# Kernel optimization log

Measured on AMD Instinct MI355X. Metric: run time of the kernel, lower is better.

Reference implementation:

```python
import jax, jax.numpy as jnp
import numpy as np
from jax import lax

N, CIN, H, W = 128, 1024, 14, 14
CF, TH = 128, 128          # cv_filter, te_hidden
HP, GT, FP, A = 256, 256, 256, 32


def setup_inputs() -> dict:
    key = jax.random.key(0)
    ks = jax.random.split(key, 12)
    s = 0.05
    return {
        "image": jax.random.normal(ks[0], (N, CIN, H, W), jnp.float32),
        "code": jax.random.normal(ks[1], (N, TH), jnp.float32),
        "conv_w": jax.random.normal(ks[2], (CF, CIN, 3, 3), jnp.float32) * 0.02,
        "conv_b": jnp.zeros((CF,), jnp.float32),
        "hp_w0": jax.random.normal(ks[3], (CF + 2 + TH, HP), jnp.float32) * s,
        "hp_b0": jnp.zeros((HP,), jnp.float32),
        "hp_w1": jax.random.normal(ks[4], (HP, 1), jnp.float32) * s,
        "hp_b1": jnp.zeros((1,), jnp.float32),
        "gt_w0": jax.random.normal(ks[5], ((CF + 2) * 2 + TH, GT), jnp.float32) * s,
        "gt_b0": jnp.zeros((GT,), jnp.float32),
        "gt_w1": jax.random.normal(ks[6], (GT, GT), jnp.float32) * s,
        "gt_b1": jnp.zeros((GT,), jnp.float32),
        "fp_w0": jax.random.normal(ks[7], (GT, FP), jnp.float32) * s,
        "fp_b0": jnp.zeros((FP,), jnp.float32),
        "fp_w1": jax.random.normal(ks[8], (FP, A), jnp.float32) * s,
        "fp_b1": jnp.zeros((A,), jnp.float32),
    }


def _sarn(image, code, conv_w, conv_b, hp_w0, hp_b0, hp_w1, hp_b1,
          gt_w0, gt_b0, gt_w1, gt_b1, fp_w0, fp_b0, fp_w1, fp_b1):
    # visual_resize: 3x3 conv, stride 1, pad 1 (NCHW)
    x = lax.conv_general_dilated(image, conv_w, (1, 1), "SAME",
                                 dimension_numbers=("NCHW", "OIHW", "NCHW"))
    x = x + conv_b[None, :, None, None]                       # [n, cf, h, w]
    n, c, h, w = x.shape
    o = h * w
    # sarn_encode: append x/y coordinate channels and question code
    xc = jnp.broadcast_to(jnp.linspace(-1.0, 1.0, h).reshape(1, 1, h, 1), (n, 1, h, w))
    yc = jnp.broadcast_to(jnp.linspace(-1.0, 1.0, w).reshape(1, 1, 1, w), (n, 1, h, w))
    coord = jnp.concatenate([x, xc, yc], axis=1)              # [n, cf+2, h, w]
    q = jnp.broadcast_to(code[:, :, None, None], (n, code.shape[1], h, w))
    qenc = jnp.concatenate([coord, q], axis=1)                # [n, cf+2+th, h, w]
    ce = coord.reshape(n, c + 2, o).transpose(0, 2, 1)        # [n, o, cf+2]
    qe = qenc.reshape(n, -1, o).transpose(0, 2, 1)            # [n, o, cf+2+th]
    # h_psi: per-object attention logit
    a = jax.nn.relu(jnp.einsum("nod,dh->noh", qe, hp_w0) + hp_b0)
    att = jnp.einsum("noh,hk->nok", a, hp_w1) + hp_b1         # [n, o, 1]
    # sarn_pair: softmax select a single soft object, pair with every object
    sel = jax.nn.softmax(att[..., 0], axis=1)                 # [n, o]
    selected = jnp.einsum("no,nod->nd", sel, ce)              # [n, cf+2]
    pairs = jnp.concatenate(
        [qe, jnp.broadcast_to(selected[:, None, :], ce.shape)], axis=2)  # [n, o, 2*(cf+2)+th]
    # g_theta MLP + sum over objects
    g = jax.nn.relu(jnp.einsum("nop,pg->nog", pairs, gt_w0) + gt_b0)
    g = jax.nn.relu(jnp.einsum("nog,gk->nok", g, gt_w1) + gt_b1)
    relations = g.sum(axis=1)                                 # [n, gt]
    # f_phi MLP -> answer logits
    f = jax.nn.relu(relations @ fp_w0 + fp_b0)
    return f @ fp_w1 + fp_b1                                  # [n, a_size]


def reference(image, code, conv_w, conv_b, hp_w0, hp_b0, hp_w1, hp_b1,
              gt_w0, gt_b0, gt_w1, gt_b1, fp_w0, fp_b0, fp_w1, fp_b1):
    return _sarn(image, code, conv_w, conv_b, hp_w0, hp_b0, hp_w1, hp_b1,
                 gt_w0, gt_b0, gt_w1, gt_b1, fp_w0, fp_b0, fp_w1, fp_b1)
```

## Files before the change

kernel.cpp:

```cpp
#include <hip/hip_runtime.h>
#include <stdint.h>

typedef unsigned short u16;
typedef __bf16 bf16x8 __attribute__((ext_vector_type(8)));
typedef float f32x4 __attribute__((ext_vector_type(4)));

__device__ __forceinline__ u16 f2b(float f) {
  union { float f; uint32_t u; } v; v.f = f;
  uint32_t r = v.u + 0x7fffu + ((v.u >> 16) & 1u);
  return (u16)(r >> 16);
}
__device__ __forceinline__ float b2f(u16 b) {
  union { float f; uint32_t u; } v; v.u = ((uint32_t)b) << 16;
  return v.f;
}
__device__ __forceinline__ void g2l16(const void* g, void* l) {
  __builtin_amdgcn_global_load_lds(
      (const __attribute__((address_space(1))) void*)g,
      (__attribute__((address_space(3))) void*)l, 16, 0, 0);
}

#define N_SAMP 128
#define OPAD   224
#define ROWS   (N_SAMP * OPAD)

__global__ __launch_bounds__(256) void prep_weights(
    const float* __restrict__ conv_w, const float* __restrict__ hp_w0,
    const float* __restrict__ gt_w0, const float* __restrict__ gt_w1,
    u16* __restrict__ W2, u16* __restrict__ hp_w0t,
    u16* __restrict__ gt_w0t, u16* __restrict__ gt_w1t) {
  int idx = blockIdx.x * 256 + threadIdx.x;
  const int nW2 = 9 * 128 * 1024;
  const int nHP = 256 * 288;
  const int nGT0 = 256 * 288;
  const int nGT1 = 256 * 256;
  if (idx < nW2) {
    int s = idx / 131072; int r = idx & 131071;
    int cf = r >> 10; int cin = r & 1023;
    W2[idx] = f2b(conv_w[(cf * 1024 + cin) * 9 + s]);
    return;
  }
  idx -= nW2;
  if (idx < nHP) {
    int nn = idx / 288, kk = idx % 288;
    hp_w0t[nn * 288 + kk] = (kk < 258) ? f2b(hp_w0[kk * 256 + nn]) : (u16)0;
    return;
  }
  idx -= nHP;
  if (idx < nGT0) {
    int nn = idx / 288, kk = idx % 288;
    gt_w0t[nn * 288 + kk] = (kk < 258) ? f2b(gt_w0[kk * 256 + nn]) : (u16)0;
    return;
  }
  idx -= nGT0;
  if (idx < nGT1) {
    int nn = idx >> 8, kk = idx & 255;
    gt_w1t[nn * 256 + kk] = f2b(gt_w1[kk * 256 + nn]);
  }
}

__global__ __launch_bounds__(256) void prep_img(const float* __restrict__ image,
                                                u16* __restrict__ imgT) {
  __shared__ float t[64][197];
  int n = blockIdx.x >> 4;
  int cin0 = (blockIdx.x & 15) * 64;
  const float* src = image + ((size_t)n * 1024 + cin0) * 196;
  for (int e = threadIdx.x; e < 64 * 196; e += 256) {
    int c = e / 196, sp = e % 196;
    t[c][sp] = src[c * 196 + sp];
  }
  __syncthreads();
  int w = threadIdx.x >> 6, lane = threadIdx.x & 63;
  for (int i = 0; i < 64; ++i) {
    int spg = i * 4 + w;
    int gy = spg >> 4, gx = spg & 15;
    float v = 0.f;
    if (gy >= 1 && gy <= 14 && gx >= 1 && gx <= 14) v = t[lane][(gy - 1) * 14 + (gx - 1)];
    imgT[(((size_t)(n * 256 + spg)) << 10) + cin0 + lane] = f2b(v);
  }
}

__global__ __launch_bounds__(256) void fill_qe(const float* __restrict__ code,
                                               u16* __restrict__ qeb) {
  int base = blockIdx.x * 8;
  for (int rr = 0; rr < 8; ++rr) {
    int r = base + rr;
    int n = r / 224, o = r % 224;
    int y = o / 14, x = o % 14;
    bool valid = o < 196;
    u16* row = qeb + (size_t)r * 288;
    for (int c = threadIdx.x; c < 288; c += 256) {
      u16 v;
      if (c < 128) { if (valid) continue; v = 0; }
      else if (c == 128) v = valid ? f2b(-1.f + 2.f * y / 13.f) : (u16)0;
      else if (c == 129) v = valid ? f2b(-1.f + 2.f * x / 13.f) : (u16)0;
      else if (c < 258) v = valid ? f2b(code[n * 128 + (c - 130)]) : (u16)0;
      else v = 0;
      row[c] = v;
    }
  }
}

__global__ __launch_bounds__(256) void conv_gemm(
    const u16* __restrict__ imgT, const u16* __restrict__ W2,
    float* __restrict__ convAcc) {
  __shared__ __align__(16) u16 lA[2][128 * 64];
  __shared__ __align__(16) u16 lB[2][128 * 64];
  int tid = threadIdx.x, lane = tid & 63, w = tid >> 6;
  int wg = blockIdx.x;
  int xcd = wg & 7, grp = wg >> 3;
  int n = ((grp / 6) << 3) | xcd;
  int r6 = grp % 6;
  int oh = r6 / 3, ks = r6 % 3;
  int oBase = oh * 112;
  size_t nBase = (size_t)n << 8;
  int rowIn = lane >> 3;
  int cA = ((lane & 7) ^ rowIn) << 3;

  int yxA[4];
  for (int ii = 0; ii < 4; ++ii) {
    int t = w + ii * 4;
    int o = oBase + t * 8 + rowIn;
    bool valid = (o < 196) && (t < 14);
    int y = o / 14, x = o - y * 14;
    yxA[ii] = valid ? (y * 16 + x) : 0;
  }

  f32x4 acc[7][2];
#pragma unroll
  for (int mt = 0; mt < 7; ++mt)
#pragma unroll
    for (int j = 0; j < 2; ++j) acc[mt][j] = (f32x4){0.f, 0.f, 0.f, 0.f};

  int l = lane & 15, q = lane >> 4;

  auto STAGE = [&](int buf, int si, int k0) {
    int off = ks * 16 + si;
    const u16* Ws = W2 + ((size_t)((ks * 3 + si) * 128) << 10);
#pragma unroll
    for (int ii = 0; ii < 4; ++ii)
      g2l16(imgT + ((nBase + (size_t)(yxA[ii] + off)) << 10) + k0 + cA,
            &lA[buf][(w + ii * 4) * 512]);
#pragma unroll
    for (int ii = 0; ii < 4; ++ii)
      g2l16(Ws + ((size_t)((w + ii * 4) * 8 + rowIn) << 10) + k0 + cA,
            &lB[buf][(w + ii * 4) * 512]);
  };

  auto COMPUTE = [&](int cur) {
#pragma unroll
    for (int kk = 0; kk < 2; ++kk) {
      int co = ((((kk << 2) | q) ^ (l & 7)) << 3);
      bf16x8 af[7];
#pragma unroll
      for (int mt = 0; mt < 7; ++mt)
        af[mt] = *(const bf16x8*)&lA[cur][(mt * 16 + l) * 64 + co];
#pragma unroll
      for (int jj = 0; jj < 2; ++jj) {
        bf16x8 bb = *(const bf16x8*)&lB[cur][(w * 32 + jj * 16 + l) * 64 + co];
#pragma unroll
        for (int mt = 0; mt < 7; ++mt)
          acc[mt][jj] = __builtin_amdgcn_mfma_f32_16x16x32_bf16(af[mt], bb, acc[mt][jj], 0, 0, 0);
      }
    }
  };

  STAGE(0, 0, 0);
#pragma unroll 2
  for (int it = 0; it < 47; ++it) {
    int nxt = it + 1;
    STAGE(nxt & 1, nxt >> 4, (nxt & 15) << 6);
    asm volatile("s_waitcnt vmcnt(8)" ::: "memory");
    __builtin_amdgcn_s_barrier();
    __builtin_amdgcn_sched_barrier(0);
    COMPUTE(it & 1);
    __builtin_amdgcn_sched_barrier(0);
    __builtin_amdgcn_s_barrier();
    __builtin_amdgcn_sched_barrier(0);
  }
  asm volatile("s_waitcnt vmcnt(0)" ::: "memory");
  __builtin_amdgcn_s_barrier();
  __builtin_amdgcn_sched_barrier(0);
  COMPUTE(1);

#pragma unroll
  for (int mt = 0; mt < 7; ++mt) {
    int o = oBase + mt * 16 + q * 4;
#pragma unroll
    for (int r4 = 0; r4 < 4; ++r4) {
      if (o + r4 < 196) {
        float* dst = convAcc + (size_t)(n * 224 + o + r4) * 128 + w * 32 + l;
        atomicAdd(dst, acc[mt][0][r4]);
        atomicAdd(dst + 16, acc[mt][1][r4]);
      }
    }
  }
}

__global__ __launch_bounds__(256) void conv_fix(
    const float* __restrict__ convAcc, const float* __restrict__ conv_b,
    u16* __restrict__ qeb) {
  int idx = blockIdx.x * 256 + threadIdx.x;
  int row196 = idx >> 5;
  int c0 = (idx & 31) << 2;
  int n = row196 / 196, o = row196 - n * 196;
  size_t row = (size_t)(n * 224 + o);
  const float4 v = *(const float4*)(convAcc + (row << 7) + c0);
  const float4 b = *(const float4*)(conv_b + c0);
  ushort4 pk;
  pk.x = f2b(v.x + b.x); pk.y = f2b(v.y + b.y);
  pk.z = f2b(v.z + b.z); pk.w = f2b(v.w + b.w);
  *(ushort4*)(qeb + row * 288 + c0) = pk;
}

template <int MODE, int KP, int KC>
__global__ __launch_bounds__(256) void gemm_kernel(
    const u16* __restrict__ A, const u16* __restrict__ Bt,
    const float* __restrict__ bias, const float* __restrict__ vec,
    float* __restrict__ outF, u16* __restrict__ outB) {
  __shared__ __align__(16) u16 lA[2][128 * 32];
  __shared__ __align__(16) u16 lB[2][128 * 32];
  int tid = threadIdx.x, lane = tid & 63, w = tid >> 6;
  int bx = blockIdx.x, by = blockIdx.y;
  int r0 = bx * 112;
  int cBase = by * 128;
  int kb = (((lane & 3) ^ ((lane >> 3) & 3)) << 3);
  int rA0 = r0 + w * 16 + (lane >> 2);
  int rA1 = r0 + (w + 4) * 16 + (lane >> 2);
  const u16* gA0 = A + (size_t)rA0 * KP + kb;
  const u16* gA1 = A + (size_t)rA1 * KP + kb;
  int cB0 = cBase + w * 16 + (lane >> 2);
  int cB1 = cBase + (w + 4) * 16 + (lane >> 2);
  const u16* gB0 = Bt + (size_t)cB0 * KP + kb;
  const u16* gB1 = Bt + (size_t)cB1 * KP + kb;

  f32x4 acc[7][2];
#pragma unroll
  for (int mt = 0; mt < 7; ++mt)
#pragma unroll
    for (int j = 0; j < 2; ++j) acc[mt][j] = (f32x4){0.f, 0.f, 0.f, 0.f};
  int colW = w * 32;
  int l = lane & 15, q = lane >> 4;
  int co = ((q ^ ((l >> 1) & 3)) << 3);

  auto STAGE = [&](int buf, int cb) {
    g2l16(gA0 + cb * 32, &lA[buf][w * 512]);
    g2l16(gA1 + cb * 32, &lA[buf][(w + 4) * 512]);
    g2l16(gB0 + cb * 32, &lB[buf][w * 512]);
    g2l16(gB1 + cb * 32, &lB[buf][(w + 4) * 512]);
  };

  auto COMPUTE = [&](int cur) {
    bf16x8 af[7];
#pragma unroll
    for (int mt = 0; mt < 7; ++mt)
      af[mt] = *(const bf16x8*)&lA[cur][(mt * 16 + l) * 32 + co];
#pragma unroll
    for (int j = 0; j < 2; ++j) {
      bf16x8 bfr = *(const bf16x8*)&lB[cur][(colW + j * 16 + l) * 32 + co];
#pragma unroll
      for (int mt = 0; mt < 7; ++mt)
        acc[mt][j] = __builtin_amdgcn_mfma_f32_16x16x32_bf16(af[mt], bfr, acc[mt][j], 0, 0, 0);
    }
  };

  STAGE(0, 0);
#pragma unroll
  for (int it = 0; it < KC - 1; ++it) {
    STAGE((it & 1) ^ 1, it + 1);
    asm volatile("s_waitcnt vmcnt(4)" ::: "memory");
    __builtin_amdgcn_s_barrier();
    __builtin_amdgcn_sched_barrier(0);
    COMPUTE(it & 1);
    __builtin_amdgcn_sched_barrier(0);
    __builtin_amdgcn_s_barrier();
    __builtin_amdgcn_sched_barrier(0);
  }
  asm volatile("s_waitcnt vmcnt(0)" ::: "memory");
  __builtin_amdgcn_s_barrier();
  __builtin_amdgcn_sched_barrier(0);
  COMPUTE((KC - 1) & 1);

  int q4 = lane >> 4, c = lane & 15;
  if (MODE == 0) {
    float attp[7][4];
#pragma unroll
    for (int mt = 0; mt < 7; ++mt)
#pragma unroll
      for (int r = 0; r < 4; ++r) attp[mt][r] = 0.f;
#pragma unroll
    for (int j = 0; j < 2; ++j) {
      int col = cBase + colW + j * 16 + c;
      float b0 = bias[col], w1 = vec[col];
#pragma unroll
      for (int mt = 0; mt < 7; ++mt)
#pragma unroll
        for (int r = 0; r < 4; ++r) {
          float v = fmaxf(acc[mt][j][r] + b0, 0.f);
          attp[mt][r] += v * w1;
        }
    }
#pragma unroll
    for (int mt = 0; mt < 7; ++mt)
#pragma unroll
      for (int r = 0; r < 4; ++r) {
        float p = attp[mt][r];
        p += __shfl_xor(p, 1, 64);
        p += __shfl_xor(p, 2, 64);
        p += __shfl_xor(p, 4, 64);
        p += __shfl_xor(p, 8, 64);
        if (c == 0) atomicAdd(&outF[r0 + mt * 16 + q4 * 4 + r], p);
      }
  } else if (MODE == 1) {
    int n = bx >> 1;
#pragma unroll
    for (int mt = 0; mt < 7; ++mt)
#pragma unroll
      for (int j = 0; j < 2; ++j) {
        int col = cBase + colW + j * 16 + c;
        float b = bias[n * 256 + col];
#pragma unroll
        for (int r = 0; r < 4; ++r) {
          int row = r0 + mt * 16 + q4 * 4 + r;
          outB[(size_t)row * 256 + col] = f2b(fmaxf(acc[mt][j][r] + b, 0.f));
        }
      }
  } else {
    int n = bx >> 1;
    int ob = (bx & 1) * 112;
#pragma unroll
    for (int j = 0; j < 2; ++j) {
      int col = cBase + colW + j * 16 + c;
      float b = bias[col];
      float sum = 0.f;
#pragma unroll
      for (int mt = 0; mt < 7; ++mt)
#pragma unroll
        for (int r = 0; r < 4; ++r) {
          int o = ob + mt * 16 + q4 * 4 + r;
          if (o < 196) sum += fmaxf(acc[mt][j][r] + b, 0.f);
        }
      sum += __shfl_xor(sum, 16, 64);
      sum += __shfl_xor(sum, 32, 64);
      if (q4 == 0) atomicAdd(&outF[n * 256 + col], sum);
    }
  }
}

__global__ __launch_bounds__(256) void sel_kernel(
    const float* __restrict__ att, const u16* __restrict__ qeb,
    const float* __restrict__ gt_w0, const float* __restrict__ gt_b0,
    float* __restrict__ bias2) {
  int n = blockIdx.x, t = threadIdx.x;
  int w = t >> 6, lane = t & 63;
  __shared__ u16 sq[196][130];
  __shared__ float sm[196];
  __shared__ float sel[130];
  __shared__ float red[8];
  const u16* base = qeb + (size_t)n * 224 * 288;
  for (int o = w; o < 196; o += 4) {
    const u16* rowp = base + (size_t)o * 288;
    for (int c = lane; c < 130; c += 64) sq[o][c] = rowp[c];
  }
  float a = (t < 196) ? att[n * 224 + t] : -1e30f;
  float m = a;
  for (int mask = 1; mask < 64; mask <<= 1) m = fmaxf(m, __shfl_xor(m, mask, 64));
  if (lane == 0) red[w] = m;
  __syncthreads();
  float M = fmaxf(fmaxf(red[0], red[1]), fmaxf(red[2], red[3]));
  float e = (t < 196) ? expf(a - M) : 0.f;
  float sAcc = e;
  for (int mask = 1; mask < 64; mask <<= 1) sAcc += __shfl_xor(sAcc, mask, 64);
  if (lane == 0) red[4 + w] = sAcc;
  __syncthreads();
  float S = red[4] + red[5] + red[6] + red[7];
  if (t < 196) sm[t] = e / S;
  __syncthreads();
  if (t < 130) {
    float acc = 0.f;
    for (int o = 0; o < 196; ++o) acc += sm[o] * b2f(sq[o][t]);
    sel[t] = acc;
  }
  __syncthreads();
  float acc2 = gt_b0[t];
  for (int d = 0; d < 130; ++d) acc2 += sel[d] * gt_w0[(258 + d) * 256 + t];
  bias2[n * 256 + t] = acc2;
}

__global__ __launch_bounds__(256) void fphi(
    const float* __restrict__ relations, const float* __restrict__ fp_w0,
    const float* __restrict__ fp_b0, const float* __restrict__ fp_w1,
    const float* __restrict__ fp_b1, float* __restrict__ out) {
  int n = blockIdx.x, t = threadIdx.x;
  __shared__ float rel[256];
  __shared__ float f[256];
  rel[t] = relations[n * 256 + t];
  __syncthreads();
  float acc = fp_b0[t];
  for (int k = 0; k < 256; ++k) acc += rel[k] * fp_w0[k * 256 + t];
  f[t] = fmaxf(acc, 0.f);
  __syncthreads();
  if (t < 32) {
    float o = fp_b1[0];
    for (int k = 0; k < 256; ++k) o += f[k] * fp_w1[k * 32 + t];
    out[n * 32 + t] = o;
  }
}

extern "C" void kernel_launch(void* const* d_in, const int* in_sizes, int n_in,
                              void* d_out, int out_size, void* d_ws, size_t ws_size,
                              hipStream_t stream) {
  const float* image = (const float*)d_in[0];
  const float* code = (const float*)d_in[1];
  const float* conv_w = (const float*)d_in[2];
  const float* conv_b = (const float*)d_in[3];
  const float* hp_w0 = (const float*)d_in[4];
  const float* hp_b0 = (const float*)d_in[5];
  const float* hp_w1 = (const float*)d_in[6];
  const float* gt_w0 = (const float*)d_in[8];
  const float* gt_b0 = (const float*)d_in[9];
  const float* gt_w1 = (const float*)d_in[10];
  const float* gt_b1 = (const float*)d_in[11];
  const float* fp_w0 = (const float*)d_in[12];
  const float* fp_b0 = (const float*)d_in[13];
  const float* fp_w1 = (const float*)d_in[14];
  const float* fp_b1 = (const float*)d_in[15];
  float* out = (float*)d_out;

  char* p = (char*)d_ws;
  u16* imgT = (u16*)p;   p += (size_t)128 * 256 * 1024 * 2;
  u16* W2 = (u16*)p;     p += (size_t)9 * 128 * 1024 * 2;
  u16* qeb = (u16*)p;    p += (size_t)ROWS * 288 * 2;
  u16* hp_w0t = (u16*)p; p += (size_t)256 * 288 * 2;
  u16* gt_w0t = (u16*)p; p += (size_t)256 * 288 * 2;
  u16* gt_w1t = (u16*)p; p += (size_t)256 * 256 * 2;
  float* att = (float*)p;   p += (size_t)ROWS * 4;
  float* bias2 = (float*)p; p += (size_t)128 * 256 * 4;
  float* convAcc = (float*)p; p += (size_t)ROWS * 128 * 4;
  float* relations = (float*)p; p += (size_t)128 * 256 * 4;
  u16* g1 = (u16*)convAcc;

  hipMemsetAsync(att, 0, (size_t)ROWS * 4, stream);
  hipMemsetAsync(relations, 0, (size_t)128 * 256 * 4, stream);
  hipMemsetAsync(convAcc, 0, (size_t)ROWS * 128 * 4, stream);

  prep_weights<<<5440, 256, 0, stream>>>(conv_w, hp_w0, gt_w0, gt_w1, W2, hp_w0t, gt_w0t, gt_w1t);
  prep_img<<<2048, 256, 0, stream>>>(image, imgT);
  fill_qe<<<ROWS / 8, 256, 0, stream>>>(code, qeb);
  conv_gemm<<<768, 256, 0, stream>>>(imgT, W2, convAcc);
  conv_fix<<<3136, 256, 0, stream>>>(convAcc, conv_b, qeb);
  gemm_kernel<0, 288, 9><<<dim3(256, 2), 256, 0, stream>>>(qeb, hp_w0t, hp_b0, hp_w1, att, nullptr);
  sel_kernel<<<128, 256, 0, stream>>>(att, qeb, gt_w0, gt_b0, bias2);
  gemm_kernel<1, 288, 9><<<dim3(256, 2), 256, 0, stream>>>(qeb, gt_w0t, bias2, nullptr, nullptr, g1);
  gemm_kernel<2, 256, 8><<<dim3(256, 2), 256, 0, stream>>>(g1, gt_w1t, gt_b1, nullptr, relations, nullptr);
  fphi<<<128, 256, 0, stream>>>(relations, fp_w0, fp_b0, fp_w1, fp_b1, out);
}
```

Baseline: 425.7 us.

## Rework conv GEMM into 4-slot K32 pipeline with 2-way split-K

Restructures the implicit-GEMM conv kernel. The old version used a double-buffered K=64 stage across 3 tap splits (768 blocks). The new one uses a 4-slot ring of K=32 half-stages with three loads in flight, a 2-way split over the 288 half-steps (512 blocks), a new LDS swizzle, and 32-bit offset arithmetic. LDS fragment reads are issued before the next stage's loads and barrier, and MFMAs run at raised priority, so memory latency overlaps compute. The cost is more barriers per unit of K work and fewer blocks, which may lower occupancy and load balance. Fewer atomic partial-sum writes are needed.

```diff
diff --git a/kernel.cpp b/kernel.cpp
--- a/kernel.cpp
+++ b/kernel.cpp
@@ -104,26 +104,28 @@
 __global__ __launch_bounds__(256) void conv_gemm(
     const u16* __restrict__ imgT, const u16* __restrict__ W2,
     float* __restrict__ convAcc) {
-  __shared__ __align__(16) u16 lA[2][128 * 64];
-  __shared__ __align__(16) u16 lB[2][128 * 64];
+  __shared__ __align__(16) u16 lA[4 * 4096];
+  __shared__ __align__(16) u16 lB[4 * 4096];
   int tid = threadIdx.x, lane = tid & 63, w = tid >> 6;
   int wg = blockIdx.x;
   int xcd = wg & 7, grp = wg >> 3;
-  int n = ((grp / 6) << 3) | xcd;
-  int r6 = grp % 6;
-  int oh = r6 / 3, ks = r6 % 3;
+  int n = ((grp >> 2) << 3) | xcd;
+  int r4g = grp & 3;
+  int oh = r4g >> 1, ks = r4g & 1;
   int oBase = oh * 112;
-  size_t nBase = (size_t)n << 8;
-  int rowIn = lane >> 3;
-  int cA = ((lane & 7) ^ rowIn) << 3;
-
-  int yxA[4];
-  for (int ii = 0; ii < 4; ++ii) {
+  int nBase = n << 8;
+  int rowIn = lane >> 2;
+  int swz = (((lane & 3) ^ ((lane >> 3) & 3)) << 3);
+
+  int aLane[2], bLane[2];
+  for (int ii = 0; ii < 2; ++ii) {
     int t = w + ii * 4;
-    int o = oBase + t * 8 + rowIn;
-    bool valid = (o < 196) && (t < 14);
+    int o = oBase + t * 16 + rowIn;
+    bool valid = (o < 196) && (t < 7);
     int y = o / 14, x = o - y * 14;
-    yxA[ii] = valid ? (y * 16 + x) : 0;
+    int yx = valid ? (y * 16 + x) : 0;
+    aLane[ii] = (yx << 10) + swz;
+    bLane[ii] = ((t * 16 + rowIn) << 10) + swz;
   }
 
   f32x4 acc[7][2];
@@ -133,55 +135,64 @@
     for (int j = 0; j < 2; ++j) acc[mt][j] = (f32x4){0.f, 0.f, 0.f, 0.f};
 
   int l = lane & 15, q = lane >> 4;
-
-  auto STAGE = [&](int buf, int si, int k0) {
-    int off = ks * 16 + si;
-    const u16* Ws = W2 + ((size_t)((ks * 3 + si) * 128) << 10);
-#pragma unroll
-    for (int ii = 0; ii < 4; ++ii)
-      g2l16(imgT + ((nBase + (size_t)(yxA[ii] + off)) << 10) + k0 + cA,
-            &lA[buf][(w + ii * 4) * 512]);
-#pragma unroll
-    for (int ii = 0; ii < 4; ++ii)
-      g2l16(Ws + ((size_t)((w + ii * 4) * 8 + rowIn) << 10) + k0 + cA,
-            &lB[buf][(w + ii * 4) * 512]);
+  int co = ((q ^ ((l >> 1) & 3)) << 3);
+  int hBase = ks * 144;
+
+  auto STAGE = [&](int slot, int h) {
+    int hg = hBase + h;
+    int s = hg >> 1;
+    int tap = s >> 4, cb = s & 15, kk = hg & 1;
+    int colb = (cb << 6) + (kk << 5);
+    int d3 = tap / 3;
+    int aScal = ((nBase + d3 * 16 + (tap - d3 * 3)) << 10) + colb;
+    int bScal = ((tap << 17) ) + colb;
+#pragma unroll
+    for (int ii = 0; ii < 2; ++ii)
+      g2l16(imgT + (size_t)aScal + aLane[ii], &lA[slot * 4096 + (w + ii * 4) * 512]);
+#pragma unroll
+    for (int ii = 0; ii < 2; ++ii)
+      g2l16(W2 + (size_t)bScal + bLane[ii], &lB[slot * 4096 + (w + ii * 4) * 512]);
   };
 
-  auto COMPUTE = [&](int cur) {
-#pragma unroll
-    for (int kk = 0; kk < 2; ++kk) {
-      int co = ((((kk << 2) | q) ^ (l & 7)) << 3);
-      bf16x8 af[7];
-#pragma unroll
-      for (int mt = 0; mt < 7; ++mt)
-        af[mt] = *(const bf16x8*)&lA[cur][(mt * 16 + l) * 64 + co];
-#pragma unroll
-      for (int jj = 0; jj < 2; ++jj) {
-        bf16x8 bb = *(const bf16x8*)&lB[cur][(w * 32 + jj * 16 + l) * 64 + co];
-#pragma unroll
-        for (int mt = 0; mt < 7; ++mt)
-          acc[mt][jj] = __builtin_amdgcn_mfma_f32_16x16x32_bf16(af[mt], bb, acc[mt][jj], 0, 0, 0);
-      }
-    }
-  };
-
-  STAGE(0, 0, 0);
-#pragma unroll 2
-  for (int it = 0; it < 47; ++it) {
-    int nxt = it + 1;
-    STAGE(nxt & 1, nxt >> 4, (nxt & 15) << 6);
-    asm volatile("s_waitcnt vmcnt(8)" ::: "memory");
-    __builtin_amdgcn_s_barrier();
-    __builtin_amdgcn_sched_barrier(0);
-    COMPUTE(it & 1);
-    __builtin_amdgcn_sched_barrier(0);
-    __builtin_amdgcn_s_barrier();
-    __builtin_amdgcn_sched_barrier(0);
-  }
-  asm volatile("s_waitcnt vmcnt(0)" ::: "memory");
+  STAGE(0, 0);
+  STAGE(1, 1);
+  STAGE(2, 2);
+  asm volatile("s_waitcnt vmcnt(8)" ::: "memory");
   __builtin_amdgcn_s_barrier();
   __builtin_amdgcn_sched_barrier(0);
-  COMPUTE(1);
+
+#pragma unroll 4
+  for (int h = 0; h < 144; ++h) {
+    int slot = h & 3;
+    const u16* aS = lA + slot * 4096;
+    const u16* bS = lB + slot * 4096;
+    bf16x8 af[7], bb0, bb1;
+#pragma unroll
+    for (int mt = 0; mt < 7; ++mt)
+      af[mt] = *(const bf16x8*)&aS[(mt * 16 + l) * 32 + co];
+    bb0 = *(const bf16x8*)&bS[(w * 32 + l) * 32 + co];
+    bb1 = *(const bf16x8*)&bS[(w * 32 + 16 + l) * 32 + co];
+    if (h <= 140) {
+      STAGE((h + 3) & 3, h + 3);
+      asm volatile("s_waitcnt vmcnt(8)" ::: "memory");
+    } else {
+      asm volatile("s_waitcnt vmcnt(0)" ::: "memory");
+    }
+    __builtin_amdgcn_s_barrier();
+    asm volatile("s_waitcnt lgkmcnt(0)" ::: "memory");
+    __builtin_amdgcn_sched_barrier(0);
+    __builtin_amdgcn_s_setprio(1);
+#pragma unroll
+    for (int mt = 0; mt < 7; ++mt)
+      acc[mt][0] = __builtin_amdgcn_mfma_f32_16x16x32_bf16(af[mt], bb0, acc[mt][0], 0, 0, 0);
+#pragma unroll
+    for (int mt = 0; mt < 7; ++mt)
+      acc[mt][1] = __builtin_amdgcn_mfma_f32_16x16x32_bf16(af[mt], bb1, acc[mt][1], 0, 0, 0);
+    __builtin_amdgcn_s_setprio(0);
+    __builtin_amdgcn_sched_barrier(0);
+    __builtin_amdgcn_s_barrier();
+    __builtin_amdgcn_sched_barrier(0);
+  }
 
 #pragma unroll
   for (int mt = 0; mt < 7; ++mt) {
@@ -447,7 +458,7 @@
   prep_weights<<<5440, 256, 0, stream>>>(conv_w, hp_w0, gt_w0, gt_w1, W2, hp_w0t, gt_w0t, gt_w1t);
   prep_img<<<2048, 256, 0, stream>>>(image, imgT);
   fill_qe<<<ROWS / 8, 256, 0, stream>>>(code, qeb);
-  conv_gemm<<<768, 256, 0, stream>>>(imgT, W2, convAcc);
+  conv_gemm<<<512, 256, 0, stream>>>(imgT, W2, convAcc);
   conv_fix<<<3136, 256, 0, stream>>>(convAcc, conv_b, qeb);
   gemm_kernel<0, 288, 9><<<dim3(256, 2), 256, 0, stream>>>(qeb, hp_w0t, hp_b0, hp_w1, att, nullptr);
   sel_kernel<<<128, 256, 0, stream>>>(att, qeb, gt_w0, gt_b0, bias2);
```

Measured after the change: 423.4 us. No clear change (-0.5%).

## Restructure conv GEMM to reuse padded image tile across all nine taps

Applied to the files above, without the earlier changes.

The conv implicit-GEMM now loads the whole padded 16x16 image plane for a 32-channel slice into LDS once and reuses it for all 9 filter taps by shifting the row offset. Only weight tiles are streamed, through a 4-slot ring. Each block covers all 196 output positions and all 128 filters, and the work is split 4 ways along input channels instead of 3 ways by tap, so the grid drops from 768 to 512 blocks. This is meant to cut redundant image loads from global memory. In exchange there are more atomic adds per block, one barrier per 32-wide k step, and a hand-tuned waitcnt schedule that is fragile.

```diff
diff --git a/kernel.cpp b/kernel.cpp
--- a/kernel.cpp
+++ b/kernel.cpp
@@ -104,94 +104,116 @@
 __global__ __launch_bounds__(256) void conv_gemm(
     const u16* __restrict__ imgT, const u16* __restrict__ W2,
     float* __restrict__ convAcc) {
-  __shared__ __align__(16) u16 lA[2][128 * 64];
-  __shared__ __align__(16) u16 lB[2][128 * 64];
+  __shared__ __align__(16) u16 lA[2][256 * 32];
+  __shared__ __align__(16) u16 lB[4][128 * 32];
   int tid = threadIdx.x, lane = tid & 63, w = tid >> 6;
   int wg = blockIdx.x;
-  int xcd = wg & 7, grp = wg >> 3;
-  int n = ((grp / 6) << 3) | xcd;
-  int r6 = grp % 6;
-  int oh = r6 / 3, ks = r6 % 3;
-  int oBase = oh * 112;
+  int xcd = wg & 7;
+  int ks = xcd >> 1;
+  int n = ((wg >> 3) << 1) | (xcd & 1);
+  int kbase = ks << 3;
   size_t nBase = (size_t)n << 8;
-  int rowIn = lane >> 3;
-  int cA = ((lane & 7) ^ rowIn) << 3;
-
-  int yxA[4];
-  for (int ii = 0; ii < 4; ++ii) {
-    int t = w + ii * 4;
-    int o = oBase + t * 8 + rowIn;
-    bool valid = (o < 196) && (t < 14);
+  int wm = w >> 1, wn = w & 1;
+  int rowIn = lane >> 2;
+  int swz = (((lane & 3) ^ ((rowIn >> 1) & 3)) << 3);
+
+  int l = lane & 15, q = lane >> 4;
+
+  int posB[7];
+#pragma unroll
+  for (int mt = 0; mt < 7; ++mt) {
+    int o = wm * 112 + mt * 16 + l;
     int y = o / 14, x = o - y * 14;
-    yxA[ii] = valid ? (y * 16 + x) : 0;
-  }
-
-  f32x4 acc[7][2];
+    posB[mt] = (o < 196) ? (y * 16 + x) : 0;
+  }
+
+  f32x4 acc[7][4];
 #pragma unroll
   for (int mt = 0; mt < 7; ++mt)
 #pragma unroll
-    for (int j = 0; j < 2; ++j) acc[mt][j] = (f32x4){0.f, 0.f, 0.f, 0.f};
-
-  int l = lane & 15, q = lane >> 4;
-
-  auto STAGE = [&](int buf, int si, int k0) {
-    int off = ks * 16 + si;
-    const u16* Ws = W2 + ((size_t)((ks * 3 + si) * 128) << 10);
-#pragma unroll
-    for (int ii = 0; ii < 4; ++ii)
-      g2l16(imgT + ((nBase + (size_t)(yxA[ii] + off)) << 10) + k0 + cA,
-            &lA[buf][(w + ii * 4) * 512]);
-#pragma unroll
-    for (int ii = 0; ii < 4; ++ii)
-      g2l16(Ws + ((size_t)((w + ii * 4) * 8 + rowIn) << 10) + k0 + cA,
-            &lB[buf][(w + ii * 4) * 512]);
+    for (int j = 0; j < 4; ++j) acc[mt][j] = (f32x4){0.f, 0.f, 0.f, 0.f};
+
+  auto STAGE_A = [&](int buf, int cbg) {
+    int k0 = cbg << 5;
+#pragma unroll
+    for (int ii = 0; ii < 4; ++ii) {
+      int r = w * 64 + ii * 16;
+      g2l16(imgT + ((nBase + (size_t)(r + rowIn)) << 10) + k0 + swz,
+            &lA[buf][r * 32]);
+    }
   };
-
-  auto COMPUTE = [&](int cur) {
-#pragma unroll
-    for (int kk = 0; kk < 2; ++kk) {
-      int co = ((((kk << 2) | q) ^ (l & 7)) << 3);
-      bf16x8 af[7];
-#pragma unroll
-      for (int mt = 0; mt < 7; ++mt)
-        af[mt] = *(const bf16x8*)&lA[cur][(mt * 16 + l) * 64 + co];
-#pragma unroll
-      for (int jj = 0; jj < 2; ++jj) {
-        bf16x8 bb = *(const bf16x8*)&lB[cur][(w * 32 + jj * 16 + l) * 64 + co];
-#pragma unroll
-        for (int mt = 0; mt < 7; ++mt)
-          acc[mt][jj] = __builtin_amdgcn_mfma_f32_16x16x32_bf16(af[mt], bb, acc[mt][jj], 0, 0, 0);
-      }
+  auto STAGE_B = [&](int slot, int ss) {
+    int cbg = kbase + ss / 9;
+    int tp = ss - (ss / 9) * 9;
+    int k0 = cbg << 5;
+    const u16* Ws = W2 + (((size_t)tp * 128) << 10);
+#pragma unroll
+    for (int ii = 0; ii < 2; ++ii) {
+      int c = w * 32 + ii * 16;
+      g2l16(Ws + ((size_t)(c + rowIn) << 10) + k0 + swz, &lB[slot][c * 32]);
     }
   };
 
-  STAGE(0, 0, 0);
-#pragma unroll 2
-  for (int it = 0; it < 47; ++it) {
-    int nxt = it + 1;
-    STAGE(nxt & 1, nxt >> 4, (nxt & 15) << 6);
-    asm volatile("s_waitcnt vmcnt(8)" ::: "memory");
+  STAGE_A(0, kbase);
+  STAGE_B(0, 0);
+  STAGE_B(1, 1);
+
+  int tap = 0, tapOff = 0, cb = 0;
+#pragma unroll 1
+  for (int s = 0; s < 72; ++s) {
+    if (s + 2 < 72) STAGE_B((s + 2) & 3, s + 2);
+    if (tap == 7 && cb < 7) STAGE_A((cb + 1) & 1, kbase + cb + 1);
+    if (s < 68) {
+      if (tap >= 7) asm volatile("s_waitcnt vmcnt(8)" ::: "memory");
+      else          asm volatile("s_waitcnt vmcnt(4)" ::: "memory");
+    } else if (s < 70) {
+      asm volatile("s_waitcnt vmcnt(4)" ::: "memory");
+    } else if (s == 70) {
+      asm volatile("s_waitcnt vmcnt(2)" ::: "memory");
+    } else {
+      asm volatile("s_waitcnt vmcnt(0)" ::: "memory");
+    }
     __builtin_amdgcn_s_barrier();
     __builtin_amdgcn_sched_barrier(0);
-    COMPUTE(it & 1);
-    __builtin_amdgcn_sched_barrier(0);
-    __builtin_amdgcn_s_barrier();
-    __builtin_amdgcn_sched_barrier(0);
-  }
-  asm volatile("s_waitcnt vmcnt(0)" ::: "memory");
-  __builtin_amdgcn_s_barrier();
-  __builtin_amdgcn_sched_barrier(0);
-  COMPUTE(1);
+
+    const char* aS = (const char*)lA[cb & 1];
+    const char* bS = (const char*)lB[s & 3];
+    bf16x8 af[7], bf[4];
+#pragma unroll
+    for (int mt = 0; mt < 7; ++mt) {
+      int r = posB[mt] + tapOff;
+      af[mt] = *(const bf16x8*)(aS + (r << 6) + (((q ^ (r >> 1)) & 3) << 4));
+    }
+#pragma unroll
+    for (int j = 0; j < 4; ++j) {
+      int rc = wn * 64 + j * 16 + l;
+      bf[j] = *(const bf16x8*)(bS + (rc << 6) + (((q ^ (rc >> 1)) & 3) << 4));
+    }
+    asm volatile("s_waitcnt lgkmcnt(0)" ::: "memory");
+    __builtin_amdgcn_sched_barrier(0);
+    __builtin_amdgcn_s_setprio(1);
+#pragma unroll
+    for (int mt = 0; mt < 7; ++mt)
+#pragma unroll
+      for (int j = 0; j < 4; ++j)
+        acc[mt][j] = __builtin_amdgcn_mfma_f32_16x16x32_bf16(af[mt], bf[j], acc[mt][j], 0, 0, 0);
+    __builtin_amdgcn_s_setprio(0);
+    __builtin_amdgcn_sched_barrier(0);
+
+    if (++tap == 9) { tap = 0; tapOff = 0; ++cb; }
+    else tapOff += ((tap == 3) | (tap == 6)) ? 14 : 1;
+  }
 
 #pragma unroll
   for (int mt = 0; mt < 7; ++mt) {
-    int o = oBase + mt * 16 + q * 4;
-#pragma unroll
-    for (int r4 = 0; r4 < 4; ++r4) {
-      if (o + r4 < 196) {
-        float* dst = convAcc + (size_t)(n * 224 + o + r4) * 128 + w * 32 + l;
-        atomicAdd(dst, acc[mt][0][r4]);
-        atomicAdd(dst + 16, acc[mt][1][r4]);
+    int o = wm * 112 + mt * 16 + q * 4;
+#pragma unroll
+    for (int j = 0; j < 4; ++j) {
+      int col = wn * 64 + j * 16 + l;
+#pragma unroll
+      for (int r4 = 0; r4 < 4; ++r4) {
+        if (o + r4 < 196)
+          atomicAdd(convAcc + (size_t)(n * 224 + o + r4) * 128 + col, acc[mt][j][r4]);
       }
     }
   }
@@ -447,7 +469,7 @@
   prep_weights<<<5440, 256, 0, stream>>>(conv_w, hp_w0, gt_w0, gt_w1, W2, hp_w0t, gt_w0t, gt_w1t);
   prep_img<<<2048, 256, 0, stream>>>(image, imgT);
   fill_qe<<<ROWS / 8, 256, 0, stream>>>(code, qeb);
-  conv_gemm<<<768, 256, 0, stream>>>(imgT, W2, convAcc);
+  conv_gemm<<<512, 256, 0, stream>>>(imgT, W2, convAcc);
   conv_fix<<<3136, 256, 0, stream>>>(convAcc, conv_b, qeb);
   gemm_kernel<0, 288, 9><<<dim3(256, 2), 256, 0, stream>>>(qeb, hp_w0t, hp_b0, hp_w1, att, nullptr);
   sel_kernel<<<128, 256, 0, stream>>>(att, qeb, gt_w0, gt_b0, bias2);
```

Measured after the change: 425.4 us. About the same (-0.1%).
